# Kernel optimization log

Hardware: AMD Instinct MI355X
Metric: run time of the kernel (lower is better)

## Reference

```python
import jax, jax.numpy as jnp
import numpy as np

N_NODES = 100000
N_EDGES = 1600000
IN_F = 48
OUT_F = 48


def setup_inputs() -> dict:
    key = jax.random.key(0)
    k1, k2, k3, k4 = jax.random.split(key, 4)
    x = jax.random.normal(k1, (N_NODES, IN_F), dtype=jnp.float32)
    edge_index = jax.random.randint(k2, (2, N_EDGES), 0, N_NODES, dtype=jnp.int32)
    # nn.Linear(in_features, out_features): W is [out, in], b is [out]
    bound = 1.0 / np.sqrt(IN_F)
    W = jax.random.uniform(k3, (OUT_F, IN_F), minval=-bound, maxval=bound, dtype=jnp.float32)
    b = jax.random.uniform(k4, (OUT_F,), minval=-bound, maxval=bound, dtype=jnp.float32)
    return {"x": x, "edge_index": edge_index, "W": W, "b": b}


def reference(x, edge_index, W, b):
    row, col = edge_index[0], edge_index[1]
    n = x.shape[0]
    # degree of each node as message target (bincount over row)
    deg = jnp.bincount(row, length=n).astype(x.dtype)
    deg_inv_sqrt = jnp.where(deg > 0, jax.lax.rsqrt(jnp.where(deg > 0, deg, 1.0)), 0.0)
    norm = deg_inv_sqrt[row] * deg_inv_sqrt[col]          # [E]
    # symmetric-normalized GCN aggregation: sum over edges of norm * x[col] into row
    msg = norm[:, None] * x[col]                           # [E, in]
    agg = jax.ops.segment_sum(msg, row, num_segments=n)    # [N, in]
    out = agg @ W.T + b                                    # [N, out]
    return jax.nn.relu(out)
```

## Files before the change

### kernel.cpp

```cpp
#include <hip/hip_runtime.h>


#define NF 48
#define NPAIR 24
#define ZLD 32
#define RB 64
#define CHUNK 16384
#define SCOL_CAP 2048

typedef __attribute__((ext_vector_type(8))) short frag_ab;
typedef __attribute__((ext_vector_type(4))) float f32x4;

__device__ inline unsigned short f2bf(float f) {
    unsigned u = __float_as_uint(f);
    u = (u + 0x7fffu + ((u >> 16) & 1u)) >> 16;
    return (unsigned short)u;
}

__global__ void transform_kernel(const float* __restrict__ x, const float* __restrict__ W,
                                 const float* __restrict__ dis,
                                 unsigned short* __restrict__ zp16, int N) {
    __shared__ unsigned short Xb[64 * 64];
    __shared__ unsigned short Wb[48 * 64];
    const int tid = threadIdx.x;
    const int nb0 = blockIdx.x * 64;

    const float4* x4 = (const float4*)x;
    for (int i = tid; i < 768; i += 256) {
        int r = i / 12, c = i % 12;
        int n = nb0 + r;
        float4 v = (n < N) ? x4[(size_t)n * 12 + c] : make_float4(0.f, 0.f, 0.f, 0.f);
        unsigned short* d = &Xb[r * 64 + c * 4];
        d[0] = f2bf(v.x); d[1] = f2bf(v.y); d[2] = f2bf(v.z); d[3] = f2bf(v.w);
    }
    for (int i = tid; i < 64 * 8; i += 256)
        ((unsigned*)Xb)[(i >> 3) * 32 + 24 + (i & 7)] = 0u;
    const float4* W4 = (const float4*)W;
    for (int i = tid; i < 576; i += 256) {
        int r = i / 12, c = i % 12;
        float4 v = W4[r * 12 + c];
        unsigned short* d = &Wb[r * 64 + c * 4];
        d[0] = f2bf(v.x); d[1] = f2bf(v.y); d[2] = f2bf(v.z); d[3] = f2bf(v.w);
    }
    for (int i = tid; i < 48 * 8; i += 256)
        ((unsigned*)Wb)[(i >> 3) * 32 + 24 + (i & 7)] = 0u;
    __syncthreads();

    const int wv = tid >> 6, lane = tid & 63;
    const int quad = lane >> 4, l16 = lane & 15;
    const int mrow = wv * 16 + l16;

    frag_ab A0 = *(const frag_ab*)&Xb[mrow * 64 + quad * 8];
    frag_ab A1 = *(const frag_ab*)&Xb[mrow * 64 + 32 + quad * 8];
    f32x4 acc[3];
#pragma unroll
    for (int t = 0; t < 3; t++) {
        frag_ab B0 = *(const frag_ab*)&Wb[(t * 16 + l16) * 64 + quad * 8];
        frag_ab B1 = *(const frag_ab*)&Wb[(t * 16 + l16) * 64 + 32 + quad * 8];
        f32x4 z = {0.f, 0.f, 0.f, 0.f};
        z = __builtin_amdgcn_mfma_f32_16x16x32_bf16(A0, B0, z, 0, 0, 0);
        z = __builtin_amdgcn_mfma_f32_16x16x32_bf16(A1, B1, z, 0, 0, 0);
        acc[t] = z;
    }
#pragma unroll
    for (int r = 0; r < 4; r++) {
        int n = nb0 + wv * 16 + quad * 4 + r;
        if (n < N) {
            float dn = dis[n];
            unsigned short* zr = zp16 + (size_t)n * 64;
#pragma unroll
            for (int t = 0; t < 3; t++)
                zr[t * 16 + l16] = f2bf(dn * acc[t][r]);
            zr[48 + l16] = 0;
        }
    }
}

__global__ void histA_kernel(const int* __restrict__ row, int* __restrict__ blkhist,
                             int NBUK, int E) {
    extern __shared__ int hist[];
    for (int i = threadIdx.x; i < NBUK; i += blockDim.x) hist[i] = 0;
    __syncthreads();
    int b = blockIdx.x;
    int s = b * CHUNK, t = min(E, s + CHUNK);
    int nv = (t - s) >> 2;
    const int4* r4 = (const int4*)(row + s);
    for (int i = threadIdx.x; i < nv; i += blockDim.x) {
        int4 r = r4[i];
        atomicAdd(&hist[r.x >> 6], 1);
        atomicAdd(&hist[r.y >> 6], 1);
        atomicAdd(&hist[r.z >> 6], 1);
        atomicAdd(&hist[r.w >> 6], 1);
    }
    for (int e = s + nv * 4 + threadIdx.x; e < t; e += blockDim.x)
        atomicAdd(&hist[row[e] >> 6], 1);
    __syncthreads();
    int* dst = blkhist + (size_t)b * NBUK;
    for (int k = threadIdx.x; k < NBUK; k += blockDim.x) dst[k] = hist[k];
}

__global__ void scanB1_kernel(int* __restrict__ blkhist, int* __restrict__ btotal,
                              int NBUK, int NCH) {
    int k = blockIdx.x;
    int lane = threadIdx.x;
    int carry = 0;
    for (int base = 0; base < NCH; base += 64) {
        int i = base + lane;
        int v = (i < NCH) ? blkhist[(size_t)i * NBUK + k] : 0;
        int incl = v;
        #pragma unroll
        for (int off = 1; off < 64; off <<= 1) {
            int u = __shfl_up(incl, off, 64);
            if (lane >= off) incl += u;
        }
        if (i < NCH) blkhist[(size_t)i * NBUK + k] = carry + incl - v;
        carry += __shfl(incl, 63, 64);
    }
    if (lane == 0) btotal[k] = carry;
}

__global__ void scanB2_kernel(const int* __restrict__ btotal, int* __restrict__ bbase,
                              int NBUK, int E) {
    __shared__ int wsum[8];
    __shared__ int carry_s;
    if (threadIdx.x == 0) carry_s = 0;
    __syncthreads();
    const int lane = threadIdx.x & 63;
    const int wave = threadIdx.x >> 6;
    for (int base = 0; base < NBUK; base += 512) {
        int i = base + threadIdx.x;
        int v = (i < NBUK) ? btotal[i] : 0;
        int incl = v;
        #pragma unroll
        for (int off = 1; off < 64; off <<= 1) {
            int u = __shfl_up(incl, off, 64);
            if (lane >= off) incl += u;
        }
        if (lane == 63) wsum[wave] = incl;
        __syncthreads();
        int woff = 0;
        #pragma unroll
        for (int w = 0; w < 8; w++) if (w < wave) woff += wsum[w];
        if (i < NBUK) bbase[i] = carry_s + woff + (incl - v);
        __syncthreads();
        if (threadIdx.x == 511) carry_s += woff + incl;
        __syncthreads();
    }
    if (threadIdx.x == 0) bbase[NBUK] = E;
}

__global__ void scatC_kernel(const int* __restrict__ row, const int* __restrict__ col,
                             const int* __restrict__ blkhist, const int* __restrict__ bbase,
                             unsigned* __restrict__ binned, int NBUK, int E) {
    extern __shared__ int cur[];
    int b = blockIdx.x;
    const int* boff = blkhist + (size_t)b * NBUK;
    for (int k = threadIdx.x; k < NBUK; k += blockDim.x)
        cur[k] = bbase[k] + boff[k];
    __syncthreads();
    int s = b * CHUNK, t = min(E, s + CHUNK);
    int nv = (t - s) >> 2;
    const int4* r4 = (const int4*)(row + s);
    const int4* c4 = (const int4*)(col + s);
    for (int i = threadIdx.x; i < nv; i += blockDim.x) {
        int4 r = r4[i];
        int4 c = c4[i];
        int p0 = atomicAdd(&cur[r.x >> 6], 1);
        binned[p0] = ((unsigned)(r.x & (RB - 1)) << 26) | (unsigned)c.x;
        int p1 = atomicAdd(&cur[r.y >> 6], 1);
        binned[p1] = ((unsigned)(r.y & (RB - 1)) << 26) | (unsigned)c.y;
        int p2 = atomicAdd(&cur[r.z >> 6], 1);
        binned[p2] = ((unsigned)(r.z & (RB - 1)) << 26) | (unsigned)c.z;
        int p3 = atomicAdd(&cur[r.w >> 6], 1);
        binned[p3] = ((unsigned)(r.w & (RB - 1)) << 26) | (unsigned)c.w;
    }
    for (int e = s + nv * 4 + threadIdx.x; e < t; e += blockDim.x) {
        int r = row[e], c = col[e];
        int pos = atomicAdd(&cur[r >> 6], 1);
        binned[pos] = ((unsigned)(r & (RB - 1)) << 26) | (unsigned)c;
    }
}

__global__ void degdis_kernel(const int* __restrict__ bbase, const unsigned* __restrict__ binned,
                              float* __restrict__ dis, int* __restrict__ lrp_g, int N) {
    __shared__ int hist[RB];
    const int b = blockIdx.x;
    const int s = bbase[b];
    const int t = bbase[b + 1];
    const int tid = threadIdx.x;
    if (tid < RB) hist[tid] = 0;
    __syncthreads();
    for (int e = s + tid; e < t; e += 512)
        atomicAdd(&hist[binned[e] >> 26], 1);
    __syncthreads();
    if (tid < RB) {
        int v = hist[tid];
        int incl = v;
        #pragma unroll
        for (int off = 1; off < 64; off <<= 1) {
            int u = __shfl_up(incl, off, 64);
            if (tid >= off) incl += u;
        }
        int* lp = lrp_g + (size_t)b * (RB + 1);
        lp[tid] = incl - v;
        if (tid == RB - 1) lp[RB] = incl;
        int n = b * RB + tid;
        if (n < N) dis[n] = (v > 0) ? rsqrtf((float)v) : 0.0f;
    }
}

__global__ __launch_bounds__(512, 8)
void aggregate_kernel(const int* __restrict__ bbase, const unsigned* __restrict__ binned,
                      const int* __restrict__ lrp_g,
                      const unsigned* __restrict__ zp, const float* __restrict__ dis,
                      const float* __restrict__ bias, float* __restrict__ out, int N) {
    __shared__ int scol[SCOL_CAP];
    __shared__ int lrp[RB + 1];
    __shared__ int cur[RB];
    const int b = blockIdx.x;
    const int s = bbase[b];
    const int t = bbase[b + 1];
    const int cnt = t - s;
    const int tid = threadIdx.x;
    if (tid < RB + 1) {
        int v = lrp_g[(size_t)b * (RB + 1) + tid];
        lrp[tid] = v;
        if (tid < RB) cur[tid] = v;
    }
    __syncthreads();
    const bool sorted = (cnt <= SCOL_CAP);
    if (sorted) {
        for (int e = s + tid; e < t; e += 512) {
            unsigned rc = binned[e];
            int pos = atomicAdd(&cur[rc >> 26], 1);
            scol[pos] = (int)(rc & 0x3ffffffu);
        }
    }
    __syncthreads();

    const int lane = tid & 63;
    const int wave = tid >> 6;
    const int h = lane >> 5;
    const int j = lane & 31;
    const bool act = (j < NPAIR);
    float bb0 = 0.0f, bb1 = 0.0f;
    if (act) { bb0 = bias[2 * j]; bb1 = bias[2 * j + 1]; }
    const int rbase = b * RB;
    for (int ri = wave; ri < RB; ri += 8) {
        int r = rbase + ri;
        if (r >= N) break;
        float a0 = 0.0f, a1 = 0.0f;
        if (sorted) {
            int ks = lrp[ri], ke = lrp[ri + 1];
            int k = ks + h;
            for (; k + 6 < ke; k += 8) {
                int c0 = scol[k];
                int c1 = scol[k + 2];
                int c2 = scol[k + 4];
                int c3 = scol[k + 6];
                unsigned u0 = zp[((size_t)c0 << 5) + j];
                unsigned u1 = zp[((size_t)c1 << 5) + j];
                unsigned u2 = zp[((size_t)c2 << 5) + j];
                unsigned u3 = zp[((size_t)c3 << 5) + j];
                a0 += (__uint_as_float(u0 << 16) + __uint_as_float(u1 << 16)) +
                      (__uint_as_float(u2 << 16) + __uint_as_float(u3 << 16));
                a1 += (__uint_as_float(u0 & 0xffff0000u) + __uint_as_float(u1 & 0xffff0000u)) +
                      (__uint_as_float(u2 & 0xffff0000u) + __uint_as_float(u3 & 0xffff0000u));
            }
            for (; k < ke; k += 2) {
                int c0 = scol[k];
                unsigned u0 = zp[((size_t)c0 << 5) + j];
                a0 += __uint_as_float(u0 << 16);
                a1 += __uint_as_float(u0 & 0xffff0000u);
            }
        } else {
            for (int e = s; e < t; e++) {
                unsigned rc = binned[e];
                if ((int)(rc >> 26) == ri && h == 0 && act) {
                    unsigned u0 = zp[((size_t)(rc & 0x3ffffffu) << 5) + j];
                    a0 += __uint_as_float(u0 << 16);
                    a1 += __uint_as_float(u0 & 0xffff0000u);
                }
            }
        }
        a0 += __shfl_xor(a0, 32, 64);
        a1 += __shfl_xor(a1, 32, 64);
        if (h == 0 && act) {
            float dr = dis[r];
            float v0 = dr * a0 + bb0;
            float v1 = dr * a1 + bb1;
            float2 o;
            o.x = v0 > 0.0f ? v0 : 0.0f;
            o.y = v1 > 0.0f ? v1 : 0.0f;
            *(float2*)(out + (size_t)r * NF + 2 * j) = o;
        }
    }
}

extern "C" void kernel_launch(void* const* d_in, const int* in_sizes, int n_in,
                              void* d_out, int out_size, void* d_ws, size_t ws_size,
                              hipStream_t stream) {
    const float* x    = (const float*)d_in[0];
    const int*   ei   = (const int*)d_in[1];
    const float* W    = (const float*)d_in[2];
    const float* bias = (const float*)d_in[3];
    float* out = (float*)d_out;

    const int N = in_sizes[0] / NF;
    const int E = in_sizes[1] / 2;
    const int* row = ei;
    const int* col = ei + E;
    const int NBUK = (N + RB - 1) / RB;
    const int NCH  = (E + CHUNK - 1) / CHUNK;

    char* ws = (char*)d_ws;
    unsigned* zp      = (unsigned*)ws;       ws += (size_t)N * ZLD * 4;
    unsigned* binned  = (unsigned*)ws;       ws += (size_t)E * 4;
    float*    dis     = (float*)ws;          ws += (size_t)N * 4;
    int*      blkhist = (int*)ws;            ws += (size_t)NCH * NBUK * 4;
    int*      btotal  = (int*)ws;            ws += (size_t)NBUK * 4;
    int*      bbase   = (int*)ws;            ws += (size_t)(NBUK + 1) * 4;
    int*      lrp_g   = (int*)ws;            ws += (size_t)NBUK * (RB + 1) * 4;

    histA_kernel<<<NCH, 512, NBUK * 4, stream>>>(row, blkhist, NBUK, E);
    scanB1_kernel<<<NBUK, 64, 0, stream>>>(blkhist, btotal, NBUK, NCH);
    scanB2_kernel<<<1, 512, 0, stream>>>(btotal, bbase, NBUK, E);
    scatC_kernel<<<NCH, 512, NBUK * 4, stream>>>(row, col, blkhist, bbase, binned, NBUK, E);
    degdis_kernel<<<NBUK, 512, 0, stream>>>(bbase, binned, dis, lrp_g, N);
    transform_kernel<<<(N + 63) / 64, 256, 0, stream>>>(x, W, dis, (unsigned short*)zp, N);
    aggregate_kernel<<<NBUK, 512, 0, stream>>>(bbase, binned, lrp_g, zp, dis, bias, out, N);
}
```

Measured before the change: 160.6 us.

## Fold degree computation into histogram pass and drop separate degdis kernel

Per-node degrees are now counted with global atomics during the bucket histogram pass, and the inverse-sqrt degree is computed in the per-bucket scan kernel. The per-bucket local row histogram and prefix that degdis produced are recomputed inside the aggregate kernel, so one launch and a full re-read of the binned edge array go away. CHUNK shrinks, which gives more histogram and scatter blocks for parallelism but makes the blkhist array and its scan longer. In exchange the histogram pass adds contended global atomics and a memset.

```diff
diff --git a/kernel.cpp b/kernel.cpp
--- a/kernel.cpp
+++ b/kernel.cpp
@@ -5,7 +5,7 @@
 #define NPAIR 24
 #define ZLD 32
 #define RB 64
-#define CHUNK 16384
+#define CHUNK 6144
 #define SCOL_CAP 2048
 
 typedef __attribute__((ext_vector_type(8))) short frag_ab;
@@ -77,7 +77,7 @@
 }
 
 __global__ void histA_kernel(const int* __restrict__ row, int* __restrict__ blkhist,
-                             int NBUK, int E) {
+                             int* __restrict__ deg, int NBUK, int E) {
     extern __shared__ int hist[];
     for (int i = threadIdx.x; i < NBUK; i += blockDim.x) hist[i] = 0;
     __syncthreads();
@@ -87,20 +87,24 @@
     const int4* r4 = (const int4*)(row + s);
     for (int i = threadIdx.x; i < nv; i += blockDim.x) {
         int4 r = r4[i];
-        atomicAdd(&hist[r.x >> 6], 1);
-        atomicAdd(&hist[r.y >> 6], 1);
-        atomicAdd(&hist[r.z >> 6], 1);
-        atomicAdd(&hist[r.w >> 6], 1);
-    }
-    for (int e = s + nv * 4 + threadIdx.x; e < t; e += blockDim.x)
-        atomicAdd(&hist[row[e] >> 6], 1);
+        atomicAdd(&hist[r.x >> 6], 1);  atomicAdd(&deg[r.x], 1);
+        atomicAdd(&hist[r.y >> 6], 1);  atomicAdd(&deg[r.y], 1);
+        atomicAdd(&hist[r.z >> 6], 1);  atomicAdd(&deg[r.z], 1);
+        atomicAdd(&hist[r.w >> 6], 1);  atomicAdd(&deg[r.w], 1);
+    }
+    for (int e = s + nv * 4 + threadIdx.x; e < t; e += blockDim.x) {
+        int r = row[e];
+        atomicAdd(&hist[r >> 6], 1);
+        atomicAdd(&deg[r], 1);
+    }
     __syncthreads();
     int* dst = blkhist + (size_t)b * NBUK;
     for (int k = threadIdx.x; k < NBUK; k += blockDim.x) dst[k] = hist[k];
 }
 
 __global__ void scanB1_kernel(int* __restrict__ blkhist, int* __restrict__ btotal,
-                              int NBUK, int NCH) {
+                              const int* __restrict__ deg, float* __restrict__ dis,
+                              int NBUK, int NCH, int N) {
     int k = blockIdx.x;
     int lane = threadIdx.x;
     int carry = 0;
@@ -117,6 +121,11 @@
         carry += __shfl(incl, 63, 64);
     }
     if (lane == 0) btotal[k] = carry;
+    int n = k * RB + lane;
+    if (n < N) {
+        int d = deg[n];
+        dis[n] = (d > 0) ? rsqrtf((float)d) : 0.0f;
+    }
 }
 
 __global__ void scanB2_kernel(const int* __restrict__ btotal, int* __restrict__ bbase,
@@ -181,12 +190,18 @@
     }
 }
 
-__global__ void degdis_kernel(const int* __restrict__ bbase, const unsigned* __restrict__ binned,
-                              float* __restrict__ dis, int* __restrict__ lrp_g, int N) {
+__global__ __launch_bounds__(512, 8)
+void aggregate_kernel(const int* __restrict__ bbase, const unsigned* __restrict__ binned,
+                      const unsigned* __restrict__ zp, const float* __restrict__ dis,
+                      const float* __restrict__ bias, float* __restrict__ out, int N) {
+    __shared__ int scol[SCOL_CAP];
     __shared__ int hist[RB];
+    __shared__ int lrp[RB + 1];
+    __shared__ int cur[RB];
     const int b = blockIdx.x;
     const int s = bbase[b];
     const int t = bbase[b + 1];
+    const int cnt = t - s;
     const int tid = threadIdx.x;
     if (tid < RB) hist[tid] = 0;
     __syncthreads();
@@ -201,31 +216,9 @@
             int u = __shfl_up(incl, off, 64);
             if (tid >= off) incl += u;
         }
-        int* lp = lrp_g + (size_t)b * (RB + 1);
-        lp[tid] = incl - v;
-        if (tid == RB - 1) lp[RB] = incl;
-        int n = b * RB + tid;
-        if (n < N) dis[n] = (v > 0) ? rsqrtf((float)v) : 0.0f;
-    }
-}
-
-__global__ __launch_bounds__(512, 8)
-void aggregate_kernel(const int* __restrict__ bbase, const unsigned* __restrict__ binned,
-                      const int* __restrict__ lrp_g,
-                      const unsigned* __restrict__ zp, const float* __restrict__ dis,
-                      const float* __restrict__ bias, float* __restrict__ out, int N) {
-    __shared__ int scol[SCOL_CAP];
-    __shared__ int lrp[RB + 1];
-    __shared__ int cur[RB];
-    const int b = blockIdx.x;
-    const int s = bbase[b];
-    const int t = bbase[b + 1];
-    const int cnt = t - s;
-    const int tid = threadIdx.x;
-    if (tid < RB + 1) {
-        int v = lrp_g[(size_t)b * (RB + 1) + tid];
-        lrp[tid] = v;
-        if (tid < RB) cur[tid] = v;
+        lrp[tid] = incl - v;
+        cur[tid] = incl - v;
+        if (tid == RB - 1) lrp[RB] = incl;
     }
     __syncthreads();
     const bool sorted = (cnt <= SCOL_CAP);
@@ -317,16 +310,16 @@
     unsigned* zp      = (unsigned*)ws;       ws += (size_t)N * ZLD * 4;
     unsigned* binned  = (unsigned*)ws;       ws += (size_t)E * 4;
     float*    dis     = (float*)ws;          ws += (size_t)N * 4;
+    int*      deg     = (int*)ws;            ws += (size_t)N * 4;
     int*      blkhist = (int*)ws;            ws += (size_t)NCH * NBUK * 4;
     int*      btotal  = (int*)ws;            ws += (size_t)NBUK * 4;
     int*      bbase   = (int*)ws;            ws += (size_t)(NBUK + 1) * 4;
-    int*      lrp_g   = (int*)ws;            ws += (size_t)NBUK * (RB + 1) * 4;
-
-    histA_kernel<<<NCH, 512, NBUK * 4, stream>>>(row, blkhist, NBUK, E);
-    scanB1_kernel<<<NBUK, 64, 0, stream>>>(blkhist, btotal, NBUK, NCH);
+
+    hipMemsetAsync(deg, 0, (size_t)N * 4, stream);
+    histA_kernel<<<NCH, 512, NBUK * 4, stream>>>(row, blkhist, deg, NBUK, E);
+    scanB1_kernel<<<NBUK, 64, 0, stream>>>(blkhist, btotal, deg, dis, NBUK, NCH, N);
     scanB2_kernel<<<1, 512, 0, stream>>>(btotal, bbase, NBUK, E);
     scatC_kernel<<<NCH, 512, NBUK * 4, stream>>>(row, col, blkhist, bbase, binned, NBUK, E);
-    degdis_kernel<<<NBUK, 512, 0, stream>>>(bbase, binned, dis, lrp_g, N);
     transform_kernel<<<(N + 63) / 64, 256, 0, stream>>>(x, W, dis, (unsigned short*)zp, N);
-    aggregate_kernel<<<NBUK, 512, 0, stream>>>(bbase, binned, lrp_g, zp, dis, bias, out, N);
-}
+    aggregate_kernel<<<NBUK, 512, 0, stream>>>(bbase, binned, zp, dis, bias, out, N);
+}
```

Result: slower. 236.5 us (+47.3%).

## Fuse degree normalization into bf16 transform kernel and pack rows to 96 bytes

Applied to the files above, without the earlier changes.

Merges the degree/dis kernel with the MFMA feature transform, so each 64-row bucket computes its degree histogram, normalization and transformed bf16 rows in one launch and reads dis from shared memory. This removes one kernel launch and one global round trip of dis. The transformed feature table row stride drops from 128 to 96 bytes, cutting gather traffic and footprint in aggregation. Column indices are premultiplied by the stride in shared memory. Rows no longer start on 128-byte boundaries, so each gathered row may touch an extra cache line.

```diff
diff --git a/kernel.cpp b/kernel.cpp
--- a/kernel.cpp
+++ b/kernel.cpp
@@ -3,7 +3,7 @@
 
 #define NF 48
 #define NPAIR 24
-#define ZLD 32
+#define ZLD 24
 #define RB 64
 #define CHUNK 16384
 #define SCOL_CAP 2048
@@ -15,65 +15,6 @@
     unsigned u = __float_as_uint(f);
     u = (u + 0x7fffu + ((u >> 16) & 1u)) >> 16;
     return (unsigned short)u;
-}
-
-__global__ void transform_kernel(const float* __restrict__ x, const float* __restrict__ W,
-                                 const float* __restrict__ dis,
-                                 unsigned short* __restrict__ zp16, int N) {
-    __shared__ unsigned short Xb[64 * 64];
-    __shared__ unsigned short Wb[48 * 64];
-    const int tid = threadIdx.x;
-    const int nb0 = blockIdx.x * 64;
-
-    const float4* x4 = (const float4*)x;
-    for (int i = tid; i < 768; i += 256) {
-        int r = i / 12, c = i % 12;
-        int n = nb0 + r;
-        float4 v = (n < N) ? x4[(size_t)n * 12 + c] : make_float4(0.f, 0.f, 0.f, 0.f);
-        unsigned short* d = &Xb[r * 64 + c * 4];
-        d[0] = f2bf(v.x); d[1] = f2bf(v.y); d[2] = f2bf(v.z); d[3] = f2bf(v.w);
-    }
-    for (int i = tid; i < 64 * 8; i += 256)
-        ((unsigned*)Xb)[(i >> 3) * 32 + 24 + (i & 7)] = 0u;
-    const float4* W4 = (const float4*)W;
-    for (int i = tid; i < 576; i += 256) {
-        int r = i / 12, c = i % 12;
-        float4 v = W4[r * 12 + c];
-        unsigned short* d = &Wb[r * 64 + c * 4];
-        d[0] = f2bf(v.x); d[1] = f2bf(v.y); d[2] = f2bf(v.z); d[3] = f2bf(v.w);
-    }
-    for (int i = tid; i < 48 * 8; i += 256)
-        ((unsigned*)Wb)[(i >> 3) * 32 + 24 + (i & 7)] = 0u;
-    __syncthreads();
-
-    const int wv = tid >> 6, lane = tid & 63;
-    const int quad = lane >> 4, l16 = lane & 15;
-    const int mrow = wv * 16 + l16;
-
-    frag_ab A0 = *(const frag_ab*)&Xb[mrow * 64 + quad * 8];
-    frag_ab A1 = *(const frag_ab*)&Xb[mrow * 64 + 32 + quad * 8];
-    f32x4 acc[3];
-#pragma unroll
-    for (int t = 0; t < 3; t++) {
-        frag_ab B0 = *(const frag_ab*)&Wb[(t * 16 + l16) * 64 + quad * 8];
-        frag_ab B1 = *(const frag_ab*)&Wb[(t * 16 + l16) * 64 + 32 + quad * 8];
-        f32x4 z = {0.f, 0.f, 0.f, 0.f};
-        z = __builtin_amdgcn_mfma_f32_16x16x32_bf16(A0, B0, z, 0, 0, 0);
-        z = __builtin_amdgcn_mfma_f32_16x16x32_bf16(A1, B1, z, 0, 0, 0);
-        acc[t] = z;
-    }
-#pragma unroll
-    for (int r = 0; r < 4; r++) {
-        int n = nb0 + wv * 16 + quad * 4 + r;
-        if (n < N) {
-            float dn = dis[n];
-            unsigned short* zr = zp16 + (size_t)n * 64;
-#pragma unroll
-            for (int t = 0; t < 3; t++)
-                zr[t * 16 + l16] = f2bf(dn * acc[t][r]);
-            zr[48 + l16] = 0;
-        }
-    }
 }
 
 __global__ void histA_kernel(const int* __restrict__ row, int* __restrict__ blkhist,
@@ -181,18 +122,47 @@
     }
 }
 
-__global__ void degdis_kernel(const int* __restrict__ bbase, const unsigned* __restrict__ binned,
-                              float* __restrict__ dis, int* __restrict__ lrp_g, int N) {
+__global__ __launch_bounds__(512)
+void distrans_kernel(const int* __restrict__ bbase, const unsigned* __restrict__ binned,
+                     const float* __restrict__ x, const float* __restrict__ W,
+                     float* __restrict__ dis, int* __restrict__ lrp_g,
+                     unsigned short* __restrict__ zp16, int N) {
     __shared__ int hist[RB];
+    __shared__ float disS[RB];
+    __shared__ unsigned short Xb[64 * 64];
+    __shared__ unsigned short Wb[48 * 64];
     const int b = blockIdx.x;
+    const int tid = threadIdx.x;
+    const int nb0 = b * RB;
     const int s = bbase[b];
     const int t = bbase[b + 1];
-    const int tid = threadIdx.x;
+
     if (tid < RB) hist[tid] = 0;
     __syncthreads();
     for (int e = s + tid; e < t; e += 512)
         atomicAdd(&hist[binned[e] >> 26], 1);
-    __syncthreads();
+
+    const float4* x4 = (const float4*)x;
+    for (int i = tid; i < 768; i += 512) {
+        int r = i / 12, c = i % 12;
+        int n = nb0 + r;
+        float4 v = (n < N) ? x4[(size_t)n * 12 + c] : make_float4(0.f, 0.f, 0.f, 0.f);
+        unsigned short* d = &Xb[r * 64 + c * 4];
+        d[0] = f2bf(v.x); d[1] = f2bf(v.y); d[2] = f2bf(v.z); d[3] = f2bf(v.w);
+    }
+    for (int i = tid; i < 64 * 8; i += 512)
+        ((unsigned*)Xb)[(i >> 3) * 32 + 24 + (i & 7)] = 0u;
+    const float4* W4 = (const float4*)W;
+    for (int i = tid; i < 576; i += 512) {
+        int r = i / 12, c = i % 12;
+        float4 v = W4[r * 12 + c];
+        unsigned short* d = &Wb[r * 64 + c * 4];
+        d[0] = f2bf(v.x); d[1] = f2bf(v.y); d[2] = f2bf(v.z); d[3] = f2bf(v.w);
+    }
+    for (int i = tid; i < 48 * 8; i += 512)
+        ((unsigned*)Wb)[(i >> 3) * 32 + 24 + (i & 7)] = 0u;
+    __syncthreads();
+
     if (tid < RB) {
         int v = hist[tid];
         int incl = v;
@@ -204,8 +174,42 @@
         int* lp = lrp_g + (size_t)b * (RB + 1);
         lp[tid] = incl - v;
         if (tid == RB - 1) lp[RB] = incl;
-        int n = b * RB + tid;
-        if (n < N) dis[n] = (v > 0) ? rsqrtf((float)v) : 0.0f;
+        float dv = (v > 0) ? rsqrtf((float)v) : 0.0f;
+        disS[tid] = dv;
+        int n = nb0 + tid;
+        if (n < N) dis[n] = dv;
+    }
+    __syncthreads();
+
+    if (tid < 256) {
+        const int wv = tid >> 6, lane = tid & 63;
+        const int quad = lane >> 4, l16 = lane & 15;
+        const int mrow = wv * 16 + l16;
+
+        frag_ab A0 = *(const frag_ab*)&Xb[mrow * 64 + quad * 8];
+        frag_ab A1 = *(const frag_ab*)&Xb[mrow * 64 + 32 + quad * 8];
+        f32x4 acc[3];
+#pragma unroll
+        for (int tt = 0; tt < 3; tt++) {
+            frag_ab B0 = *(const frag_ab*)&Wb[(tt * 16 + l16) * 64 + quad * 8];
+            frag_ab B1 = *(const frag_ab*)&Wb[(tt * 16 + l16) * 64 + 32 + quad * 8];
+            f32x4 z = {0.f, 0.f, 0.f, 0.f};
+            z = __builtin_amdgcn_mfma_f32_16x16x32_bf16(A0, B0, z, 0, 0, 0);
+            z = __builtin_amdgcn_mfma_f32_16x16x32_bf16(A1, B1, z, 0, 0, 0);
+            acc[tt] = z;
+        }
+#pragma unroll
+        for (int r = 0; r < 4; r++) {
+            int lrow = wv * 16 + quad * 4 + r;
+            int n = nb0 + lrow;
+            if (n < N) {
+                float dn = disS[lrow];
+                unsigned short* zr = zp16 + (size_t)n * (2 * ZLD);
+#pragma unroll
+                for (int tt = 0; tt < 3; tt++)
+                    zr[tt * 16 + l16] = f2bf(dn * acc[tt][r]);
+            }
+        }
     }
 }
 
@@ -233,7 +237,7 @@
         for (int e = s + tid; e < t; e += 512) {
             unsigned rc = binned[e];
             int pos = atomicAdd(&cur[rc >> 26], 1);
-            scol[pos] = (int)(rc & 0x3ffffffu);
+            scol[pos] = (int)((rc & 0x3ffffffu) * (unsigned)ZLD);
         }
     }
     __syncthreads();
@@ -243,6 +247,7 @@
     const int h = lane >> 5;
     const int j = lane & 31;
     const bool act = (j < NPAIR);
+    const int ja = act ? j : 0;
     float bb0 = 0.0f, bb1 = 0.0f;
     if (act) { bb0 = bias[2 * j]; bb1 = bias[2 * j + 1]; }
     const int rbase = b * RB;
@@ -258,10 +263,10 @@
                 int c1 = scol[k + 2];
                 int c2 = scol[k + 4];
                 int c3 = scol[k + 6];
-                unsigned u0 = zp[((size_t)c0 << 5) + j];
-                unsigned u1 = zp[((size_t)c1 << 5) + j];
-                unsigned u2 = zp[((size_t)c2 << 5) + j];
-                unsigned u3 = zp[((size_t)c3 << 5) + j];
+                unsigned u0 = zp[(size_t)c0 + ja];
+                unsigned u1 = zp[(size_t)c1 + ja];
+                unsigned u2 = zp[(size_t)c2 + ja];
+                unsigned u3 = zp[(size_t)c3 + ja];
                 a0 += (__uint_as_float(u0 << 16) + __uint_as_float(u1 << 16)) +
                       (__uint_as_float(u2 << 16) + __uint_as_float(u3 << 16));
                 a1 += (__uint_as_float(u0 & 0xffff0000u) + __uint_as_float(u1 & 0xffff0000u)) +
@@ -269,7 +274,7 @@
             }
             for (; k < ke; k += 2) {
                 int c0 = scol[k];
-                unsigned u0 = zp[((size_t)c0 << 5) + j];
+                unsigned u0 = zp[(size_t)c0 + ja];
                 a0 += __uint_as_float(u0 << 16);
                 a1 += __uint_as_float(u0 & 0xffff0000u);
             }
@@ -277,7 +282,7 @@
             for (int e = s; e < t; e++) {
                 unsigned rc = binned[e];
                 if ((int)(rc >> 26) == ri && h == 0 && act) {
-                    unsigned u0 = zp[((size_t)(rc & 0x3ffffffu) << 5) + j];
+                    unsigned u0 = zp[(size_t)(rc & 0x3ffffffu) * ZLD + ja];
                     a0 += __uint_as_float(u0 << 16);
                     a1 += __uint_as_float(u0 & 0xffff0000u);
                 }
@@ -326,7 +331,7 @@
     scanB1_kernel<<<NBUK, 64, 0, stream>>>(blkhist, btotal, NBUK, NCH);
     scanB2_kernel<<<1, 512, 0, stream>>>(btotal, bbase, NBUK, E);
     scatC_kernel<<<NCH, 512, NBUK * 4, stream>>>(row, col, blkhist, bbase, binned, NBUK, E);
-    degdis_kernel<<<NBUK, 512, 0, stream>>>(bbase, binned, dis, lrp_g, N);
-    transform_kernel<<<(N + 63) / 64, 256, 0, stream>>>(x, W, dis, (unsigned short*)zp, N);
+    distrans_kernel<<<NBUK, 512, 0, stream>>>(bbase, binned, x, W, dis, lrp_g,
+                                              (unsigned short*)zp, N);
     aggregate_kernel<<<NBUK, 512, 0, stream>>>(bbase, binned, lrp_g, zp, dis, bias, out, N);
 }
```

Result: no change. 159.2 us (-0.9%).
